# Kernel optimization log

Measured on AMD Instinct MI355X. Metric: run time of the kernel, lower is better.

## Reference

```python
import jax, jax.numpy as jnp
import numpy as np

D_NODE, C, N_HEAD = 64, 8, 8
LN_EPS = 1e-5
MASK_EPS = 1e-10
INF = 1e9


def setup_inputs() -> dict:
    key = jax.random.key(0)
    ks = jax.random.split(key, 12)
    B, S, R, D = 1, 2048, 384, D_NODE
    HC = N_HEAD * C
    M_raw = jax.random.normal(ks[0], (B, S, R, D), dtype=jnp.float32)
    M_mask = (jax.random.uniform(ks[1], (B, S, R)) > 0.1).astype(jnp.float32)
    sc = 1.0 / np.sqrt(D)
    return {
        "M_raw": M_raw,
        "M_mask": M_mask,
        "ln_g": jnp.ones((D,), jnp.float32),
        "ln_b": jnp.zeros((D,), jnp.float32),
        "Wq": jax.random.normal(ks[2], (D, HC), jnp.float32) * sc,
        "Wk": jax.random.normal(ks[3], (D, C), jnp.float32) * sc,
        "Wv": jax.random.normal(ks[4], (D, C), jnp.float32) * sc,
        "Wg": jax.random.normal(ks[5], (D, HC), jnp.float32) * sc,
        "bg": jnp.ones((HC,), jnp.float32),  # gating bias init to 1
        "Wo": jax.random.normal(ks[6], (HC, D), jnp.float32) * sc,
        "bo": jnp.zeros((D,), jnp.float32),
    }


def reference(M_raw, M_mask, ln_g, ln_b, Wq, Wk, Wv, Wg, bg, Wo, bo):
    # [B,S,R,D] -> [B,R,S,D]: attend over the sequence (column) axis per residue
    M = jnp.swapaxes(M_raw, -2, -3)
    mask = jnp.swapaxes(M_mask, -1, -2)  # [B,R,S]
    # LayerNorm over d_node
    mu = jnp.mean(M, axis=-1, keepdims=True)
    var = jnp.mean(jnp.square(M - mu), axis=-1, keepdims=True)
    M = (M - mu) * jax.lax.rsqrt(var + LN_EPS) * ln_g + ln_b
    # mean-pooled query over masked sequence positions -> [B,R,D]
    q_avg = jnp.sum(M * mask[..., None], axis=-2) / (jnp.sum(mask, axis=-1)[..., None] + MASK_EPS)
    q = (q_avg @ Wq).reshape(q_avg.shape[:-1] + (N_HEAD, C)) * (C ** -0.5)  # [B,R,H,c]
    k = M @ Wk  # [B,R,S,c] (shared across heads)
    v = M @ Wv  # [B,R,S,c]
    bias = (INF * (mask - 1.0))[..., None, :]  # [B,R,1,S]
    logits = jnp.einsum("brhc,brsc->brhs", q, k) + bias
    w = jax.nn.softmax(logits, axis=-1)
    o = jnp.einsum("brhs,brsc->brhc", w, v)  # [B,R,H,c]
    # per-position sigmoid gate broadcast against the single pooled output
    g = jax.nn.sigmoid(M @ Wg + bg).reshape(M.shape[:-1] + (N_HEAD, C))  # [B,R,S,H,c]
    go = (g * o[..., None, :, :]).reshape(M.shape[:-1] + (N_HEAD * C,))  # [B,R,S,H*c]
    out = go @ Wo + bo  # [B,R,S,D]
    return M_raw + jnp.swapaxes(out, -2, -3)
```

## Files before the change

### kernel.cpp

```cpp
#include <hip/hip_runtime.h>
#include <stdint.h>


#define DEV __device__ __forceinline__

typedef __attribute__((ext_vector_type(8))) short short8;
typedef __attribute__((ext_vector_type(4))) float floatx4;

static constexpr int S_DIM = 2048;
static constexpr int R_DIM = 384;

static constexpr size_t KV_OFF    = 0;
static constexpr size_t STATS_OFF = 25165824;
static constexpr size_t QPART_OFF = 31457280;
static constexpr size_t O_OFF     = 32342016;

DEV float bf2f(uint32_t u) { union { uint32_t i; float f; } c; c.i = u << 16; return c.f; }
DEV uint16_t f2bf(float f) {
  union { float f; uint32_t i; } c; c.f = f;
  return (uint16_t)((c.i + 0x7FFFu + ((c.i >> 16) & 1u)) >> 16);
}
DEV void unpack8(uint4 w, float* x) {
  x[0] = bf2f(w.x & 0xffff); x[1] = bf2f(w.x >> 16);
  x[2] = bf2f(w.y & 0xffff); x[3] = bf2f(w.y >> 16);
  x[4] = bf2f(w.z & 0xffff); x[5] = bf2f(w.z >> 16);
  x[6] = bf2f(w.w & 0xffff); x[7] = bf2f(w.w >> 16);
}
DEV uint4 pack8(const float* x) {
  uint4 w;
  w.x = (uint32_t)f2bf(x[0]) | ((uint32_t)f2bf(x[1]) << 16);
  w.y = (uint32_t)f2bf(x[2]) | ((uint32_t)f2bf(x[3]) << 16);
  w.z = (uint32_t)f2bf(x[4]) | ((uint32_t)f2bf(x[5]) << 16);
  w.w = (uint32_t)f2bf(x[6]) | ((uint32_t)f2bf(x[7]) << 16);
  return w;
}

__global__ __launch_bounds__(256) void k1_ln_kv(
    const float* __restrict__ M, const float* __restrict__ mask,
    const float* __restrict__ lng, const float* __restrict__ lnb,
    const float* __restrict__ Wk, const float* __restrict__ Wv,
    uint16_t* __restrict__ kv, float* __restrict__ stats, float* __restrict__ qpart)
{
  __shared__ float WkvL[64 * 16];
  __shared__ float lngL[64], lnbL[64];
  __shared__ float redq[4][64];
  __shared__ float redc[4];
  const int tid = threadIdx.x;
  const int r = blockIdx.y;
  const int s = blockIdx.x * 256 + tid;

  if (tid < 64) {
    lngL[tid] = lng[tid];
    lnbL[tid] = lnb[tid];
#pragma unroll
    for (int c = 0; c < 8; ++c) {
      WkvL[tid * 16 + c]     = Wk[tid * 8 + c];
      WkvL[tid * 16 + 8 + c] = Wv[tid * 8 + c];
    }
  }
  __syncthreads();

  const size_t row = (size_t)s * R_DIM + r;
  const float4* mp = (const float4*)(M + row * 64);
  float x[64];
#pragma unroll
  for (int i = 0; i < 16; ++i) {
    float4 w = mp[i];
    x[i * 4] = w.x; x[i * 4 + 1] = w.y; x[i * 4 + 2] = w.z; x[i * 4 + 3] = w.w;
  }

  float sum = 0.f, ss = 0.f;
#pragma unroll
  for (int d = 0; d < 64; ++d) { sum += x[d]; ss += x[d] * x[d]; }
  const float mu = sum * (1.f / 64.f);
  const float var = ss * (1.f / 64.f) - mu * mu;
  const float rstd = 1.f / sqrtf(var + 1e-5f);
  ((float2*)stats)[(size_t)r * S_DIM + s] = make_float2(mu, rstd);

  const float m = mask[row];
  float kp[8], vp[8];
#pragma unroll
  for (int c = 0; c < 8; ++c) { kp[c] = 0.f; vp[c] = 0.f; }
#pragma unroll
  for (int d = 0; d < 64; ++d) {
    const float xl = (x[d] - mu) * rstd * lngL[d] + lnbL[d];
    x[d] = xl * m;
#pragma unroll
    for (int c = 0; c < 8; ++c) {
      kp[c] += xl * WkvL[d * 16 + c];
      vp[c] += xl * WkvL[d * 16 + 8 + c];
    }
  }
  uint4* kvp = (uint4*)kv;
  kvp[((size_t)r * S_DIM + s) * 2]     = pack8(kp);
  kvp[((size_t)r * S_DIM + s) * 2 + 1] = pack8(vp);

  const int lane = tid & 63, wv = tid >> 6;
#pragma unroll
  for (int st = 5; st >= 0; --st) {
    const int dist = 1 << st;
    const bool hi = (lane & dist) != 0;
#pragma unroll
    for (int j = 0; j < (1 << st); ++j) {
      const float send = hi ? x[j] : x[j + dist];
      const float recv = __shfl_xor(send, dist, 64);
      x[j] = (hi ? x[j + dist] : x[j]) + recv;
    }
  }
  float cnt = m;
#pragma unroll
  for (int off = 1; off < 64; off <<= 1) cnt += __shfl_xor(cnt, off, 64);

  redq[wv][lane] = x[0];
  if (lane == 0) redc[wv] = cnt;
  __syncthreads();
  if (tid < 64)
    qpart[((size_t)r * 8 + blockIdx.x) * 72 + tid] =
        redq[0][tid] + redq[1][tid] + redq[2][tid] + redq[3][tid];
  if (tid == 64)
    qpart[((size_t)r * 8 + blockIdx.x) * 72 + 64] = redc[0] + redc[1] + redc[2] + redc[3];
}

__global__ __launch_bounds__(256) void k2_attn(
    const float* __restrict__ Wq, const float* __restrict__ mask,
    const uint16_t* __restrict__ kv, const float* __restrict__ qpart,
    float* __restrict__ oG)
{
  __shared__ float qavgL[64], qLs[64];
  __shared__ float redmax[4][8], redden[4][8], redo[4][64];
  __shared__ float cntL;
  const int tid = threadIdx.x;
  const int r = blockIdx.x;
  const int lane = tid & 63, wv = tid >> 6;

  float qs = 0.f;
  if (tid < 65) {
#pragma unroll
    for (int c = 0; c < 8; ++c) qs += qpart[((size_t)r * 8 + c) * 72 + tid];
    if (tid == 64) cntL = qs;
  }
  __syncthreads();
  if (tid < 64) qavgL[tid] = qs / (cntL + 1e-10f);
  __syncthreads();
  if (tid < 64) {
    float a = 0.f;
    for (int d = 0; d < 64; ++d) a += qavgL[d] * Wq[d * 64 + tid];
    qLs[tid] = a * 0.35355339059327373f;
  }
  __syncthreads();

  float l[64];
  float lm[8];
#pragma unroll
  for (int h = 0; h < 8; ++h) lm[h] = -3.0e38f;
  const uint4* kvp = (const uint4*)kv;
#pragma unroll
  for (int it = 0; it < 8; ++it) {
    const int s = it * 256 + tid;
    uint4 kw = kvp[((size_t)r * S_DIM + s) * 2];
    float k[8]; unpack8(kw, k);
    const float bias = (mask[(size_t)s * R_DIM + r] - 1.f) * 1e9f;
#pragma unroll
    for (int h = 0; h < 8; ++h) {
      float t = bias;
#pragma unroll
      for (int c = 0; c < 8; ++c) t += qLs[h * 8 + c] * k[c];
      l[it * 8 + h] = t;
      lm[h] = fmaxf(lm[h], t);
    }
  }
#pragma unroll
  for (int h = 0; h < 8; ++h)
#pragma unroll
    for (int off = 1; off < 64; off <<= 1) lm[h] = fmaxf(lm[h], __shfl_xor(lm[h], off, 64));
  if (lane == 0) {
#pragma unroll
    for (int h = 0; h < 8; ++h) redmax[wv][h] = lm[h];
  }
  __syncthreads();
  float gm[8];
#pragma unroll
  for (int h = 0; h < 8; ++h)
    gm[h] = fmaxf(fmaxf(redmax[0][h], redmax[1][h]), fmaxf(redmax[2][h], redmax[3][h]));

  float den[8], ao[64];
#pragma unroll
  for (int h = 0; h < 8; ++h) den[h] = 0.f;
#pragma unroll
  for (int i = 0; i < 64; ++i) ao[i] = 0.f;
#pragma unroll
  for (int it = 0; it < 8; ++it) {
    const int s = it * 256 + tid;
    uint4 vw = kvp[((size_t)r * S_DIM + s) * 2 + 1];
    float v[8]; unpack8(vw, v);
#pragma unroll
    for (int h = 0; h < 8; ++h) {
      const float w = __expf(l[it * 8 + h] - gm[h]);
      den[h] += w;
#pragma unroll
      for (int c = 0; c < 8; ++c) ao[h * 8 + c] += w * v[c];
    }
  }
#pragma unroll
  for (int st = 5; st >= 0; --st) {
    const int dist = 1 << st;
    const bool hi = (lane & dist) != 0;
#pragma unroll
    for (int j = 0; j < (1 << st); ++j) {
      const float send = hi ? ao[j] : ao[j + dist];
      const float recv = __shfl_xor(send, dist, 64);
      ao[j] = (hi ? ao[j + dist] : ao[j]) + recv;
    }
  }
#pragma unroll
  for (int h = 0; h < 8; ++h)
#pragma unroll
    for (int off = 1; off < 64; off <<= 1) den[h] += __shfl_xor(den[h], off, 64);

  redo[wv][lane] = ao[0];
  if (lane == 0) {
#pragma unroll
    for (int h = 0; h < 8; ++h) redden[wv][h] = den[h];
  }
  __syncthreads();
  if (tid < 64) {
    const float o = redo[0][tid] + redo[1][tid] + redo[2][tid] + redo[3][tid];
    const int h = tid >> 3;
    const float dd = redden[0][h] + redden[1][h] + redden[2][h] + redden[3][h];
    oG[(size_t)r * 64 + tid] = o / dd;
  }
}

__global__ __launch_bounds__(256, 2) void k3_out(
    const float* __restrict__ M, const float* __restrict__ stats,
    const float* __restrict__ oG,
    const float* __restrict__ Wg, const float* __restrict__ bg,
    const float* __restrict__ Wo, const float* __restrict__ bo,
    const float* __restrict__ lng, const float* __restrict__ lnb,
    float* __restrict__ out)
{
  constexpr int MSTR = 72;
  __shared__ uint16_t mlnL[256 * MSTR];
  __shared__ uint16_t WgT[64 * MSTR];
  __shared__ uint16_t WoT[64 * MSTR];
  __shared__ float oLs[64], lngL[64], lnbL[64];
  const int tid = threadIdx.x;
  const int r = blockIdx.y;
  const int s = blockIdx.x * 256 + tid;

#pragma unroll
  for (int i = 0; i < 16; ++i) {
    const int idx = i * 256 + tid;
    const int a = idx >> 6, b = idx & 63;
    WgT[b * MSTR + a] = f2bf(Wg[idx]);
    WoT[b * MSTR + a] = f2bf(Wo[idx]);
  }
  if (tid < 64) {
    oLs[tid] = oG[(size_t)r * 64 + tid];
    lngL[tid] = lng[tid];
    lnbL[tid] = lnb[tid];
  }
  __syncthreads();

  const size_t row = (size_t)s * R_DIM + r;
  const float4* mp = (const float4*)(M + row * 64);
  const float2 st = ((const float2*)stats)[(size_t)r * S_DIM + s];
  const float mu = st.x, rstd = st.y;
#pragma unroll
  for (int i = 0; i < 8; ++i) {
    float4 w0 = mp[i * 2], w1 = mp[i * 2 + 1];
    float yy[8] = {w0.x, w0.y, w0.z, w0.w, w1.x, w1.y, w1.z, w1.w};
#pragma unroll
    for (int u = 0; u < 8; ++u) yy[u] = (yy[u] - mu) * rstd * lngL[i * 8 + u] + lnbL[i * 8 + u];
    *(uint4*)(&mlnL[tid * MSTR + i * 8]) = pack8(yy);
  }
  __syncthreads();

  const int lane = tid & 63;
  const int wrow0 = tid & 192;
  const int mrow = lane & 15;
  const int quad = lane >> 4;

  short8 wgB[4][2], woB[4][2];
#pragma unroll
  for (int nt = 0; nt < 4; ++nt)
#pragma unroll
    for (int kk = 0; kk < 2; ++kk) {
      wgB[nt][kk] = *(const short8*)(&WgT[(nt * 16 + mrow) * MSTR + kk * 32 + quad * 8]);
      woB[nt][kk] = *(const short8*)(&WoT[(nt * 16 + mrow) * MSTR + kk * 32 + quad * 8]);
    }
  float og[4], bgr[4], bor[4];
#pragma unroll
  for (int nt = 0; nt < 4; ++nt) {
    og[nt] = oLs[nt * 16 + mrow];
    bgr[nt] = bg[nt * 16 + mrow];
    bor[nt] = bo[nt * 16 + mrow];
  }

#pragma unroll
  for (int mt = 0; mt < 4; ++mt) {
    const int arow = (wrow0 + mt * 16 + mrow) * MSTR + quad * 8;
    short8 a0 = *(const short8*)(&mlnL[arow]);
    short8 a1 = *(const short8*)(&mlnL[arow + 32]);
#pragma unroll
    for (int nt = 0; nt < 4; ++nt) {
      floatx4 c = {0.f, 0.f, 0.f, 0.f};
      c = __builtin_amdgcn_mfma_f32_16x16x32_bf16(a0, wgB[nt][0], c, 0, 0, 0);
      c = __builtin_amdgcn_mfma_f32_16x16x32_bf16(a1, wgB[nt][1], c, 0, 0, 0);
#pragma unroll
      for (int i = 0; i < 4; ++i) {
        const float z = c[i] + bgr[nt];
        const float g = 1.0f / (1.0f + __expf(-z));
        mlnL[(wrow0 + mt * 16 + quad * 4 + i) * MSTR + nt * 16 + mrow] = f2bf(g * og[nt]);
      }
    }
  }
  __syncthreads();

#pragma unroll
  for (int mt = 0; mt < 4; ++mt) {
    const int arow = (wrow0 + mt * 16 + mrow) * MSTR + quad * 8;
    short8 a0 = *(const short8*)(&mlnL[arow]);
    short8 a1 = *(const short8*)(&mlnL[arow + 32]);
#pragma unroll
    for (int nt = 0; nt < 4; ++nt) {
      floatx4 c = {0.f, 0.f, 0.f, 0.f};
      c = __builtin_amdgcn_mfma_f32_16x16x32_bf16(a0, woB[nt][0], c, 0, 0, 0);
      c = __builtin_amdgcn_mfma_f32_16x16x32_bf16(a1, woB[nt][1], c, 0, 0, 0);
#pragma unroll
      for (int i = 0; i < 4; ++i)
        mlnL[(wrow0 + mt * 16 + quad * 4 + i) * MSTR + nt * 16 + mrow] = f2bf(c[i] + bor[nt]);
    }
  }
  __syncthreads();

  float4* op = (float4*)(out + row * 64);
#pragma unroll
  for (int i = 0; i < 8; ++i) {
    float4 w0 = mp[i * 2], w1 = mp[i * 2 + 1];
    uint4 tv = *(const uint4*)(&mlnL[tid * MSTR + i * 8]);
    float yy[8]; unpack8(tv, yy);
    float4 o0 = make_float4(w0.x + yy[0], w0.y + yy[1], w0.z + yy[2], w0.w + yy[3]);
    float4 o1 = make_float4(w1.x + yy[4], w1.y + yy[5], w1.z + yy[6], w1.w + yy[7]);
    op[i * 2] = o0;
    op[i * 2 + 1] = o1;
  }
}

extern "C" void kernel_launch(void* const* d_in, const int* in_sizes, int n_in,
                              void* d_out, int out_size, void* d_ws, size_t ws_size,
                              hipStream_t stream)
{
  const float* M    = (const float*)d_in[0];
  const float* mask = (const float*)d_in[1];
  const float* lng  = (const float*)d_in[2];
  const float* lnb  = (const float*)d_in[3];
  const float* Wq   = (const float*)d_in[4];
  const float* Wk   = (const float*)d_in[5];
  const float* Wv   = (const float*)d_in[6];
  const float* Wg   = (const float*)d_in[7];
  const float* bg   = (const float*)d_in[8];
  const float* Wo   = (const float*)d_in[9];
  const float* bo   = (const float*)d_in[10];
  float* out = (float*)d_out;

  char* ws = (char*)d_ws;
  uint16_t* kvB  = (uint16_t*)(ws + KV_OFF);
  float* statsB  = (float*)(ws + STATS_OFF);
  float* qpartB  = (float*)(ws + QPART_OFF);
  float* oB      = (float*)(ws + O_OFF);

  k1_ln_kv<<<dim3(8, 384), 256, 0, stream>>>(M, mask, lng, lnb, Wk, Wv, kvB, statsB, qpartB);
  k2_attn<<<dim3(384), 256, 0, stream>>>(Wq, mask, kvB, qpartB, oB);
  k3_out<<<dim3(8, 384), 256, 0, stream>>>(M, statsB, oB, Wg, bg, Wo, bo, lng, lnb, out);
}
```

Before: 526.8 us.

## Coalesce row loads across 16 lanes and compute K/V projection with MFMA

The LayerNorm/KV kernel and the output kernel now load each 64-float row cooperatively across 16 lanes with float4 accesses, replacing one-thread-per-row strided loads. Row statistics are reduced with warp shuffles. The K/V projection moves from scalar FMAs to bf16 MFMA on a shared-memory tile, with results staged through LDS for coalesced stores. The aim is to raise global memory coalescing and cut register pressure, at the cost of extra LDS traffic, more synchronisation, and bf16 rounding of the LayerNorm output before the K/V projection.

Result: faster. 469.4 us (-10.9%).

```diff
diff --git a/kernel.cpp b/kernel.cpp
--- a/kernel.cpp
+++ b/kernel.cpp
@@ -25,14 +25,6 @@
   x[2] = bf2f(w.y & 0xffff); x[3] = bf2f(w.y >> 16);
   x[4] = bf2f(w.z & 0xffff); x[5] = bf2f(w.z >> 16);
   x[6] = bf2f(w.w & 0xffff); x[7] = bf2f(w.w >> 16);
-}
-DEV uint4 pack8(const float* x) {
-  uint4 w;
-  w.x = (uint32_t)f2bf(x[0]) | ((uint32_t)f2bf(x[1]) << 16);
-  w.y = (uint32_t)f2bf(x[2]) | ((uint32_t)f2bf(x[3]) << 16);
-  w.z = (uint32_t)f2bf(x[4]) | ((uint32_t)f2bf(x[5]) << 16);
-  w.w = (uint32_t)f2bf(x[6]) | ((uint32_t)f2bf(x[7]) << 16);
-  return w;
 }
 
 __global__ __launch_bounds__(256) void k1_ln_kv(
@@ -41,79 +33,100 @@
     const float* __restrict__ Wk, const float* __restrict__ Wv,
     uint16_t* __restrict__ kv, float* __restrict__ stats, float* __restrict__ qpart)
 {
-  __shared__ float WkvL[64 * 16];
-  __shared__ float lngL[64], lnbL[64];
+  __shared__ uint16_t mlnL[256 * 72];
+  __shared__ uint16_t WkvT[16 * 72];
+  __shared__ uint16_t kvL[256 * 16];
   __shared__ float redq[4][64];
   __shared__ float redc[4];
+
   const int tid = threadIdx.x;
   const int r = blockIdx.y;
-  const int s = blockIdx.x * 256 + tid;
-
-  if (tid < 64) {
-    lngL[tid] = lng[tid];
-    lnbL[tid] = lnb[tid];
-#pragma unroll
-    for (int c = 0; c < 8; ++c) {
-      WkvL[tid * 16 + c]     = Wk[tid * 8 + c];
-      WkvL[tid * 16 + 8 + c] = Wv[tid * 8 + c];
-    }
-  }
-  __syncthreads();
-
-  const size_t row = (size_t)s * R_DIM + r;
-  const float4* mp = (const float4*)(M + row * 64);
-  float x[64];
-#pragma unroll
-  for (int i = 0; i < 16; ++i) {
-    float4 w = mp[i];
-    x[i * 4] = w.x; x[i * 4 + 1] = w.y; x[i * 4 + 2] = w.z; x[i * 4 + 3] = w.w;
-  }
-
-  float sum = 0.f, ss = 0.f;
-#pragma unroll
-  for (int d = 0; d < 64; ++d) { sum += x[d]; ss += x[d] * x[d]; }
-  const float mu = sum * (1.f / 64.f);
-  const float var = ss * (1.f / 64.f) - mu * mu;
-  const float rstd = 1.f / sqrtf(var + 1e-5f);
-  ((float2*)stats)[(size_t)r * S_DIM + s] = make_float2(mu, rstd);
-
-  const float m = mask[row];
-  float kp[8], vp[8];
-#pragma unroll
-  for (int c = 0; c < 8; ++c) { kp[c] = 0.f; vp[c] = 0.f; }
-#pragma unroll
-  for (int d = 0; d < 64; ++d) {
-    const float xl = (x[d] - mu) * rstd * lngL[d] + lnbL[d];
-    x[d] = xl * m;
-#pragma unroll
-    for (int c = 0; c < 8; ++c) {
-      kp[c] += xl * WkvL[d * 16 + c];
-      vp[c] += xl * WkvL[d * 16 + 8 + c];
-    }
-  }
-  uint4* kvp = (uint4*)kv;
-  kvp[((size_t)r * S_DIM + s) * 2]     = pack8(kp);
-  kvp[((size_t)r * S_DIM + s) * 2 + 1] = pack8(vp);
-
-  const int lane = tid & 63, wv = tid >> 6;
-#pragma unroll
-  for (int st = 5; st >= 0; --st) {
-    const int dist = 1 << st;
-    const bool hi = (lane & dist) != 0;
-#pragma unroll
-    for (int j = 0; j < (1 << st); ++j) {
-      const float send = hi ? x[j] : x[j + dist];
-      const float recv = __shfl_xor(send, dist, 64);
-      x[j] = (hi ? x[j + dist] : x[j]) + recv;
-    }
-  }
-  float cnt = m;
-#pragma unroll
-  for (int off = 1; off < 64; off <<= 1) cnt += __shfl_xor(cnt, off, 64);
-
-  redq[wv][lane] = x[0];
-  if (lane == 0) redc[wv] = cnt;
-  __syncthreads();
+  const int s_base = blockIdx.x * 256;
+  const int w = tid >> 6, lane = tid & 63;
+  const int g = lane >> 4, c4 = lane & 15;
+
+#pragma unroll
+  for (int i = 0; i < 4; ++i) {
+    const int e = i * 256 + tid;
+    const int n = e >> 6, d = e & 63;
+    const float val = (n < 8) ? Wk[d * 8 + n] : Wv[d * 8 + (n - 8)];
+    WkvT[n * 72 + d] = f2bf(val);
+  }
+  const float4 lngv = ((const float4*)lng)[c4];
+  const float4 lnbv = ((const float4*)lnb)[c4];
+
+  float qacc[4] = {0.f, 0.f, 0.f, 0.f};
+  float cacc = 0.f;
+
+#pragma unroll
+  for (int j = 0; j < 16; ++j) {
+    const int row_local = w * 64 + j * 4 + g;
+    const int s = s_base + row_local;
+    const size_t grow = (size_t)s * R_DIM + r;
+    const float4 x = ((const float4*)(M + grow * 64))[c4];
+    float sum = x.x + x.y + x.z + x.w;
+    float ss = x.x * x.x + x.y * x.y + x.z * x.z + x.w * x.w;
+#pragma unroll
+    for (int off = 1; off < 16; off <<= 1) {
+      sum += __shfl_xor(sum, off, 64);
+      ss  += __shfl_xor(ss, off, 64);
+    }
+    const float mu = sum * (1.f / 64.f);
+    const float var = ss * (1.f / 64.f) - mu * mu;
+    const float rstd = 1.f / sqrtf(var + 1e-5f);
+    if (c4 == 0) ((float2*)stats)[(size_t)r * S_DIM + s] = make_float2(mu, rstd);
+    float y[4];
+    y[0] = (x.x - mu) * rstd * lngv.x + lnbv.x;
+    y[1] = (x.y - mu) * rstd * lngv.y + lnbv.y;
+    y[2] = (x.z - mu) * rstd * lngv.z + lnbv.z;
+    y[3] = (x.w - mu) * rstd * lngv.w + lnbv.w;
+    uint2 p;
+    p.x = (uint32_t)f2bf(y[0]) | ((uint32_t)f2bf(y[1]) << 16);
+    p.y = (uint32_t)f2bf(y[2]) | ((uint32_t)f2bf(y[3]) << 16);
+    *(uint2*)&mlnL[row_local * 72 + c4 * 4] = p;
+    const float mval = mask[grow];
+    qacc[0] += mval * y[0]; qacc[1] += mval * y[1];
+    qacc[2] += mval * y[2]; qacc[3] += mval * y[3];
+    cacc += mval;
+  }
+
+#pragma unroll
+  for (int off = 16; off < 64; off <<= 1) {
+#pragma unroll
+    for (int i = 0; i < 4; ++i) qacc[i] += __shfl_xor(qacc[i], off, 64);
+  }
+#pragma unroll
+  for (int off = 1; off < 64; off <<= 1) cacc += __shfl_xor(cacc, off, 64);
+  if (lane < 16) {
+    float4 qv = make_float4(qacc[0], qacc[1], qacc[2], qacc[3]);
+    *(float4*)&redq[w][c4 * 4] = qv;
+  }
+  if (lane == 0) redc[w] = cacc * (1.f / 16.f);
+  __syncthreads();
+
+  const short8 b0 = *(const short8*)&WkvT[c4 * 72 + g * 8];
+  const short8 b1 = *(const short8*)&WkvT[c4 * 72 + 32 + g * 8];
+#pragma unroll
+  for (int mt = 0; mt < 4; ++mt) {
+    const int brow = w * 64 + mt * 16;
+    const short8 a0 = *(const short8*)&mlnL[(brow + c4) * 72 + g * 8];
+    const short8 a1 = *(const short8*)&mlnL[(brow + c4) * 72 + 32 + g * 8];
+    floatx4 c = {0.f, 0.f, 0.f, 0.f};
+    c = __builtin_amdgcn_mfma_f32_16x16x32_bf16(a0, b0, c, 0, 0, 0);
+    c = __builtin_amdgcn_mfma_f32_16x16x32_bf16(a1, b1, c, 0, 0, 0);
+#pragma unroll
+    for (int i = 0; i < 4; ++i)
+      kvL[(brow + g * 4 + i) * 16 + c4] = f2bf(c[i]);
+  }
+  __syncthreads();
+
+#pragma unroll
+  for (int jj = 0; jj < 4; ++jj) {
+    const int row_local = w * 64 + jj * 16 + (lane >> 2);
+    const int s = s_base + row_local;
+    const uint2 val = *(const uint2*)&kvL[row_local * 16 + (lane & 3) * 4];
+    *(uint2*)(kv + ((size_t)r * S_DIM + s) * 16 + (lane & 3) * 4) = val;
+  }
   if (tid < 64)
     qpart[((size_t)r * 8 + blockIdx.x) * 72 + tid] =
         redq[0][tid] + redq[1][tid] + redq[2][tid] + redq[3][tid];
@@ -239,55 +252,57 @@
     const float* __restrict__ lng, const float* __restrict__ lnb,
     float* __restrict__ out)
 {
-  constexpr int MSTR = 72;
-  __shared__ uint16_t mlnL[256 * MSTR];
-  __shared__ uint16_t WgT[64 * MSTR];
-  __shared__ uint16_t WoT[64 * MSTR];
-  __shared__ float oLs[64], lngL[64], lnbL[64];
+  __shared__ uint16_t mlnL[256 * 72];
+  __shared__ uint16_t WgT[64 * 72];
+  __shared__ uint16_t WoT[64 * 72];
+  __shared__ float oLs[64];
   const int tid = threadIdx.x;
   const int r = blockIdx.y;
-  const int s = blockIdx.x * 256 + tid;
+  const int s_base = blockIdx.x * 256;
+  const int w = tid >> 6, lane = tid & 63;
+  const int g = lane >> 4, c4 = lane & 15;
 
 #pragma unroll
   for (int i = 0; i < 16; ++i) {
     const int idx = i * 256 + tid;
     const int a = idx >> 6, b = idx & 63;
-    WgT[b * MSTR + a] = f2bf(Wg[idx]);
-    WoT[b * MSTR + a] = f2bf(Wo[idx]);
-  }
-  if (tid < 64) {
-    oLs[tid] = oG[(size_t)r * 64 + tid];
-    lngL[tid] = lng[tid];
-    lnbL[tid] = lnb[tid];
-  }
-  __syncthreads();
-
-  const size_t row = (size_t)s * R_DIM + r;
-  const float4* mp = (const float4*)(M + row * 64);
-  const float2 st = ((const float2*)stats)[(size_t)r * S_DIM + s];
-  const float mu = st.x, rstd = st.y;
-#pragma unroll
-  for (int i = 0; i < 8; ++i) {
-    float4 w0 = mp[i * 2], w1 = mp[i * 2 + 1];
-    float yy[8] = {w0.x, w0.y, w0.z, w0.w, w1.x, w1.y, w1.z, w1.w};
-#pragma unroll
-    for (int u = 0; u < 8; ++u) yy[u] = (yy[u] - mu) * rstd * lngL[i * 8 + u] + lnbL[i * 8 + u];
-    *(uint4*)(&mlnL[tid * MSTR + i * 8]) = pack8(yy);
-  }
-  __syncthreads();
-
-  const int lane = tid & 63;
-  const int wrow0 = tid & 192;
-  const int mrow = lane & 15;
-  const int quad = lane >> 4;
+    WgT[b * 72 + a] = f2bf(Wg[idx]);
+    WoT[b * 72 + a] = f2bf(Wo[idx]);
+  }
+  if (tid < 64) oLs[tid] = oG[(size_t)r * 64 + tid];
+  const float4 lngv = ((const float4*)lng)[c4];
+  const float4 lnbv = ((const float4*)lnb)[c4];
+
+#pragma unroll
+  for (int j = 0; j < 16; ++j) {
+    const int row_local = w * 64 + j * 4 + g;
+    const int s = s_base + row_local;
+    const size_t grow = (size_t)s * R_DIM + r;
+    const float2 st = ((const float2*)stats)[(size_t)r * S_DIM + s];
+    const float4 x = ((const float4*)(M + grow * 64))[c4];
+    float y[4];
+    y[0] = (x.x - st.x) * st.y * lngv.x + lnbv.x;
+    y[1] = (x.y - st.x) * st.y * lngv.y + lnbv.y;
+    y[2] = (x.z - st.x) * st.y * lngv.z + lnbv.z;
+    y[3] = (x.w - st.x) * st.y * lngv.w + lnbv.w;
+    uint2 p;
+    p.x = (uint32_t)f2bf(y[0]) | ((uint32_t)f2bf(y[1]) << 16);
+    p.y = (uint32_t)f2bf(y[2]) | ((uint32_t)f2bf(y[3]) << 16);
+    *(uint2*)&mlnL[row_local * 72 + c4 * 4] = p;
+  }
+  __syncthreads();
+
+  const int wrow0 = w * 64;
+  const int mrow = c4;
+  const int quad = g;
 
   short8 wgB[4][2], woB[4][2];
 #pragma unroll
   for (int nt = 0; nt < 4; ++nt)
 #pragma unroll
     for (int kk = 0; kk < 2; ++kk) {
-      wgB[nt][kk] = *(const short8*)(&WgT[(nt * 16 + mrow) * MSTR + kk * 32 + quad * 8]);
-      woB[nt][kk] = *(const short8*)(&WoT[(nt * 16 + mrow) * MSTR + kk * 32 + quad * 8]);
+      wgB[nt][kk] = *(const short8*)(&WgT[(nt * 16 + mrow) * 72 + kk * 32 + quad * 8]);
+      woB[nt][kk] = *(const short8*)(&WoT[(nt * 16 + mrow) * 72 + kk * 32 + quad * 8]);
     }
   float og[4], bgr[4], bor[4];
 #pragma unroll
@@ -299,9 +314,9 @@
 
 #pragma unroll
   for (int mt = 0; mt < 4; ++mt) {
-    const int arow = (wrow0 + mt * 16 + mrow) * MSTR + quad * 8;
-    short8 a0 = *(const short8*)(&mlnL[arow]);
-    short8 a1 = *(const short8*)(&mlnL[arow + 32]);
+    const int arow = (wrow0 + mt * 16 + mrow) * 72 + quad * 8;
+    const short8 a0 = *(const short8*)(&mlnL[arow]);
+    const short8 a1 = *(const short8*)(&mlnL[arow + 32]);
 #pragma unroll
     for (int nt = 0; nt < 4; ++nt) {
       floatx4 c = {0.f, 0.f, 0.f, 0.f};
@@ -310,8 +325,8 @@
 #pragma unroll
       for (int i = 0; i < 4; ++i) {
         const float z = c[i] + bgr[nt];
-        const float g = 1.0f / (1.0f + __expf(-z));
-        mlnL[(wrow0 + mt * 16 + quad * 4 + i) * MSTR + nt * 16 + mrow] = f2bf(g * og[nt]);
+        const float gt = 1.0f / (1.0f + __expf(-z));
+        mlnL[(wrow0 + mt * 16 + quad * 4 + i) * 72 + nt * 16 + mrow] = f2bf(gt * og[nt]);
       }
     }
   }
@@ -319,9 +334,9 @@
 
 #pragma unroll
   for (int mt = 0; mt < 4; ++mt) {
-    const int arow = (wrow0 + mt * 16 + mrow) * MSTR + quad * 8;
-    short8 a0 = *(const short8*)(&mlnL[arow]);
-    short8 a1 = *(const short8*)(&mlnL[arow + 32]);
+    const int arow = (wrow0 + mt * 16 + mrow) * 72 + quad * 8;
+    const short8 a0 = *(const short8*)(&mlnL[arow]);
+    const short8 a1 = *(const short8*)(&mlnL[arow + 32]);
 #pragma unroll
     for (int nt = 0; nt < 4; ++nt) {
       floatx4 c = {0.f, 0.f, 0.f, 0.f};
@@ -329,21 +344,24 @@
       c = __builtin_amdgcn_mfma_f32_16x16x32_bf16(a1, woB[nt][1], c, 0, 0, 0);
 #pragma unroll
       for (int i = 0; i < 4; ++i)
-        mlnL[(wrow0 + mt * 16 + quad * 4 + i) * MSTR + nt * 16 + mrow] = f2bf(c[i] + bor[nt]);
-    }
-  }
-  __syncthreads();
-
-  float4* op = (float4*)(out + row * 64);
-#pragma unroll
-  for (int i = 0; i < 8; ++i) {
-    float4 w0 = mp[i * 2], w1 = mp[i * 2 + 1];
-    uint4 tv = *(const uint4*)(&mlnL[tid * MSTR + i * 8]);
-    float yy[8]; unpack8(tv, yy);
-    float4 o0 = make_float4(w0.x + yy[0], w0.y + yy[1], w0.z + yy[2], w0.w + yy[3]);
-    float4 o1 = make_float4(w1.x + yy[4], w1.y + yy[5], w1.z + yy[6], w1.w + yy[7]);
-    op[i * 2] = o0;
-    op[i * 2 + 1] = o1;
+        mlnL[(wrow0 + mt * 16 + quad * 4 + i) * 72 + nt * 16 + mrow] = f2bf(c[i] + bor[nt]);
+    }
+  }
+  __syncthreads();
+
+#pragma unroll
+  for (int j = 0; j < 16; ++j) {
+    const int row_local = w * 64 + j * 4 + g;
+    const int s = s_base + row_local;
+    const size_t grow = (size_t)s * R_DIM + r;
+    const float4 x = ((const float4*)(M + grow * 64))[c4];
+    const uint2 tv = *(const uint2*)&mlnL[row_local * 72 + c4 * 4];
+    float4 o;
+    o.x = x.x + bf2f(tv.x & 0xffff);
+    o.y = x.y + bf2f(tv.x >> 16);
+    o.z = x.z + bf2f(tv.y & 0xffff);
+    o.w = x.w + bf2f(tv.y >> 16);
+    ((float4*)(out + grow * 64))[c4] = o;
   }
 }
 
```
